# Optimization experiments

Hardware: AMD Instinct MI355X
Metric: run time of the kernel (lower is better)

The kernel has to match this reference:

```python
import jax, jax.numpy as jnp
import numpy as np

FUSE_W = 0.3
TEMP = 0.1
TOPK = 8
EPS = 1e-8


def _l2n(x, eps=EPS):
    return x / (jnp.linalg.norm(x, axis=-1, keepdims=True) + eps)


def setup_inputs() -> dict:
    key = jax.random.key(0)
    ks = jax.random.split(key, 6)
    B, Dk, Dv, N = 4096, 512, 512, 65536
    return {
        "q": jax.random.normal(ks[0], (B, Dk), jnp.float32),
        "spike_key": (jax.random.uniform(ks[1], (B, Dk)) > 0.5).astype(jnp.float32),
        "mem_keys": jax.random.normal(ks[2], (N, Dk), jnp.float32),
        "mem_values": jax.random.normal(ks[3], (N, Dv), jnp.float32),
        "W": jax.random.normal(ks[4], (Dk, Dk), jnp.float32) / np.sqrt(Dk).astype(np.float32),
        "b": jnp.zeros((Dk,), jnp.float32),
    }


def reference(q, spike_key, mem_keys, mem_values, W, b):
    # MemoryCube.query with spike fusion; memory fully filled (N = capacity).
    qn = _l2n(q)                                    # (B, Dk)
    enc = spike_key @ W.T + b                       # spike_encoder Linear
    qn = _l2n((1.0 - FUSE_W) * qn + FUSE_W * enc)   # _fuse_key
    keys_n = _l2n(mem_keys)                         # (N, Dk)
    sims = qn @ keys_n.T                            # (B, N) cosine sims
    top_vals, top_idx = jax.lax.top_k(sims, TOPK)   # (B, K)
    attn = jax.nn.softmax(top_vals / TEMP, axis=-1)
    vals = mem_values[top_idx]                      # (B, K, Dv) gather
    out = jnp.einsum('bk,bkd->bd', attn, vals)      # weighted combine
    # entropy-based confidence
    p = jnp.clip(attn, EPS, None)
    H = -(p * jnp.log(p)).sum(axis=-1)
    H_max = jnp.log(jnp.float32(TOPK))
    conf = (1.0 - H / (H_max + EPS)).mean()
    return out, conf, top_idx, attn
```

## Files before the change

### kernel.cpp

```cpp
#include <hip/hip_runtime.h>
#include <stdint.h>
#include <math.h>

typedef unsigned short u16;
typedef __attribute__((ext_vector_type(2))) float floatx2;
typedef __attribute__((ext_vector_type(4))) float floatx4;
typedef __attribute__((ext_vector_type(4))) unsigned int uintx4;
typedef __attribute__((ext_vector_type(8))) __bf16 bf16x8;

#define B_ROWS 4096
#define DK 512
#define NKEYS 65536
#define NCHUNK 32
#define CHUNK (NKEYS / NCHUNK)
#define SLOTS 32
#define CAND_PER_ROW (NCHUNK * SLOTS)
#define THRESH 0.135f

#define CONF_OFF 2097152
#define IDX_OFF  2097153
#define ATTN_OFF (IDX_OFF + B_ROWS * 8)

__device__ __forceinline__ u16 f2bf(float x) {
    union { float f; unsigned int u; } v; v.f = x;
    unsigned int r = v.u + 0x7fffu + ((v.u >> 16) & 1u);
    return (u16)(r >> 16);
}

__device__ __forceinline__ void gload_lds16(const u16* g, u16* l) {
    __builtin_amdgcn_global_load_lds(
        (const __attribute__((address_space(1))) unsigned int*)g,
        (__attribute__((address_space(3))) unsigned int*)l,
        16, 0, 0);
}

__device__ __forceinline__ float np_block128_sq(const float* a) {
#pragma clang fp contract(off)
    float r[8];
    floatx4 p0 = *(const floatx4*)&a[0];
    floatx4 p1 = *(const floatx4*)&a[4];
    r[0] = p0.x * p0.x; r[1] = p0.y * p0.y; r[2] = p0.z * p0.z; r[3] = p0.w * p0.w;
    r[4] = p1.x * p1.x; r[5] = p1.y * p1.y; r[6] = p1.z * p1.z; r[7] = p1.w * p1.w;
    for (int i = 8; i < 128; i += 8) {
        floatx4 q0 = *(const floatx4*)&a[i];
        floatx4 q1 = *(const floatx4*)&a[i + 4];
        r[0] += q0.x * q0.x; r[1] += q0.y * q0.y;
        r[2] += q0.z * q0.z; r[3] += q0.w * q0.w;
        r[4] += q1.x * q1.x; r[5] += q1.y * q1.y;
        r[6] += q1.z * q1.z; r[7] += q1.w * q1.w;
    }
    return ((r[0] + r[1]) + (r[2] + r[3])) + ((r[4] + r[5]) + (r[6] + r[7]));
}

__device__ __forceinline__ float np_sum512_sq(const float* a) {
#pragma clang fp contract(off)
    float b0 = np_block128_sq(a);
    float b1 = np_block128_sq(a + 128);
    float b2 = np_block128_sq(a + 256);
    float b3 = np_block128_sq(a + 384);
    return (b0 + b1) + (b2 + b3);
}

__device__ __forceinline__ float sqrt_f32_cr(float s) {
    return (float)sqrt((double)s);
}
__device__ __forceinline__ float div_f32_cr(float a, float b) {
    return (float)((double)a / (double)b);
}

__global__ __launch_bounds__(256) void transpose_w(const float* __restrict__ w,
                                                   float* __restrict__ wt) {
    int j = blockIdx.x, t = threadIdx.x;
    float a = w[(size_t)j * DK + t];
    float b = w[(size_t)j * DK + t + 256];
    wt[(size_t)t * DK + j] = a;
    wt[(size_t)(t + 256) * DK + j] = b;
}

__global__ __launch_bounds__(256) void prep_keys(float* __restrict__ mk,
                                                 u16* __restrict__ kbf) {
    const int row = blockIdx.x * 256 + threadIdx.x;
    float* kp = mk + (size_t)row * DK;
    float s = np_sum512_sq(kp);
    float nrm = sqrt_f32_cr(s) + 1e-8f;
    for (int i = 0; i < DK; i += 8) {
        floatx4 p0 = *(const floatx4*)&kp[i];
        floatx4 p1 = *(const floatx4*)&kp[i + 4];
        floatx4 n0, n1;
        n0.x = div_f32_cr(p0.x, nrm); n0.y = div_f32_cr(p0.y, nrm);
        n0.z = div_f32_cr(p0.z, nrm); n0.w = div_f32_cr(p0.w, nrm);
        n1.x = div_f32_cr(p1.x, nrm); n1.y = div_f32_cr(p1.y, nrm);
        n1.z = div_f32_cr(p1.z, nrm); n1.w = div_f32_cr(p1.w, nrm);
        union { uintx4 v; u16 u[8]; } pk;
        pk.u[0] = f2bf(n0.x); pk.u[1] = f2bf(n0.y);
        pk.u[2] = f2bf(n0.z); pk.u[3] = f2bf(n0.w);
        pk.u[4] = f2bf(n1.x); pk.u[5] = f2bf(n1.y);
        pk.u[6] = f2bf(n1.z); pk.u[7] = f2bf(n1.w);
        *(floatx4*)&kp[i] = n0;
        *(floatx4*)&kp[i + 4] = n1;
        *(uintx4*)&kbf[(size_t)row * DK + i] = pk.v;
    }
}

__global__ __launch_bounds__(256) void fuse_q(const float* __restrict__ q,
                                              const float* __restrict__ spike,
                                              const float* __restrict__ wt,
                                              const float* __restrict__ bvec,
                                              float* __restrict__ qn2f,
                                              u16* __restrict__ qbf) {
    __shared__ __align__(16) float s_sp[DK];
    __shared__ __align__(16) float s_q[DK];
    __shared__ __align__(16) float s_y[DK];
    __shared__ float s_nq;
    __shared__ float s_ny;
    const int t = threadIdx.x, b = blockIdx.x;
    s_sp[t] = spike[(size_t)b * DK + t];
    s_sp[t + 256] = spike[(size_t)b * DK + t + 256];
    s_q[t] = q[(size_t)b * DK + t];
    s_q[t + 256] = q[(size_t)b * DK + t + 256];
    __syncthreads();

    const int c0 = 2 * t;
    float a0 = 0.f, a1 = 0.f;
    for (int i = 0; i < DK; i += 16) {
        float sv[16]; floatx2 wv[16];
#pragma unroll
        for (int u = 0; u < 16; ++u) {
            sv[u] = s_sp[i + u];
            wv[u] = *(const floatx2*)&wt[(size_t)(i + u) * DK + c0];
        }
#pragma unroll
        for (int u = 0; u < 16; ++u) {
            a0 = fmaf(sv[u], wv[u].x, a0);
            a1 = fmaf(sv[u], wv[u].y, a1);
        }
    }

    if (t == 0) s_nq = sqrt_f32_cr(np_sum512_sq(s_q)) + 1e-8f;
    __syncthreads();
    float nq = s_nq;
    float qn0 = div_f32_cr(s_q[c0], nq);
    float qn1 = div_f32_cr(s_q[c0 + 1], nq);
    float e0 = a0 + bvec[c0];
    float e1 = a1 + bvec[c0 + 1];
    float y0, y1;
    {
#pragma clang fp contract(off)
        float u0 = 0.7f * qn0; float v0 = 0.3f * e0; y0 = u0 + v0;
        float u1 = 0.7f * qn1; float v1 = 0.3f * e1; y1 = u1 + v1;
    }
    s_y[c0] = y0; s_y[c0 + 1] = y1;
    __syncthreads();
    if (t == 0) s_ny = sqrt_f32_cr(np_sum512_sq(s_y)) + 1e-8f;
    __syncthreads();
    float ny = s_ny;
    float f0 = div_f32_cr(y0, ny);
    float f1 = div_f32_cr(y1, ny);
    *(floatx2*)&qn2f[(size_t)b * DK + c0] = (floatx2){f0, f1};
    union { unsigned int u; u16 h[2]; } pk;
    pk.h[0] = f2bf(f0); pk.h[1] = f2bf(f1);
    *(unsigned int*)&qbf[(size_t)b * DK + c0] = pk.u;
}

__global__ __launch_bounds__(256, 4) void cand_gemm(const u16* __restrict__ qbf,
                                                    const u16* __restrict__ kbf,
                                                    int* __restrict__ cidx,
                                                    int* __restrict__ gcnt) {
    __shared__ u16 ldsB[2][128 * 64];
    const int t = threadIdx.x;
    const int lane = t & 63;
    const int wave = t >> 6;
    const int qbase = blockIdx.x * 128;
    const int chunk = blockIdx.y;
    const int r0 = 64 * (wave >> 1), c0 = 64 * (wave & 1);
    const int quad = lane >> 4, m16 = lane & 15;

    const int srow = lane >> 3;
    const int scol = ((lane & 7) ^ srow) << 3;

    const u16* aRow = qbf + (size_t)(qbase + r0 + m16) * DK + quad * 8;

    floatx4 acc[4][4];

    {
        const u16* bB = kbf + (size_t)(chunk * CHUNK + wave * 32 + srow) * DK + scol;
#pragma unroll
        for (int c = 0; c < 4; ++c)
            gload_lds16(bB + (size_t)c * 8 * DK, &ldsB[0][(wave * 4 + c) * 512]);
    }
    __syncthreads();

    int cur = 0;
    for (int s = 0; s < 128; ++s) {
        const int iter = s >> 3;
        const int ks = (s & 7) << 6;
        const int nbase = chunk * CHUNK + iter * 128;

        if ((s & 7) == 0) {
#pragma unroll
            for (int i = 0; i < 4; ++i)
#pragma unroll
                for (int j = 0; j < 4; ++j) acc[i][j] = (floatx4){0.f, 0.f, 0.f, 0.f};
        }

        bf16x8 afr[2][4];
#pragma unroll
        for (int h = 0; h < 2; ++h)
#pragma unroll
            for (int i = 0; i < 4; ++i)
                afr[h][i] = __builtin_bit_cast(bf16x8,
                    *(const uintx4*)(aRow + (size_t)i * 16 * DK + ks + h * 32));

        if (s < 127) {
            const int s2 = s + 1;
            const int nb2 = chunk * CHUNK + (s2 >> 3) * 128;
            const int ks2 = (s2 & 7) << 6;
            const u16* bB = kbf + (size_t)(nb2 + wave * 32 + srow) * DK + ks2 + scol;
#pragma unroll
            for (int c = 0; c < 4; ++c)
                gload_lds16(bB + (size_t)c * 8 * DK, &ldsB[cur ^ 1][(wave * 4 + c) * 512]);
        }

#pragma unroll
        for (int h = 0; h < 2; ++h) {
            const int cb = ((h * 4 + quad) ^ (m16 & 7)) << 4;
            bf16x8 bfr[4];
#pragma unroll
            for (int j = 0; j < 4; ++j)
                bfr[j] = __builtin_bit_cast(bf16x8,
                    *(const uintx4*)((const char*)&ldsB[cur][0] + (c0 + 16 * j + m16) * 128 + cb));
#pragma unroll
            for (int i = 0; i < 4; ++i)
#pragma unroll
                for (int j = 0; j < 4; ++j)
                    acc[i][j] = __builtin_amdgcn_mfma_f32_16x16x32_bf16(
                        afr[h][i], bfr[j], acc[i][j], 0, 0, 0);
        }

        if ((s & 7) == 7) {
#pragma unroll
            for (int i = 0; i < 4; ++i)
#pragma unroll
                for (int j = 0; j < 4; ++j) {
                    int col = nbase + c0 + 16 * j + m16;
#pragma unroll
                    for (int r = 0; r < 4; ++r) {
                        float v = acc[i][j][r];
                        if (v > THRESH) {
                            int grow = qbase + r0 + 16 * i + quad * 4 + r;
                            int slot = atomicAdd(&gcnt[grow * NCHUNK + chunk], 1);
                            if (slot < SLOTS)
                                cidx[(size_t)grow * CAND_PER_ROW + chunk * SLOTS + slot] = col;
                        }
                    }
                }
        }
        __syncthreads();
        cur ^= 1;
    }
}

__global__ __launch_bounds__(256) void finalize_rows(const int* __restrict__ cidx,
                                                     const int* __restrict__ gcnt,
                                                     const float* __restrict__ qn2f,
                                                     const float* __restrict__ keys_n,
                                                     const float* __restrict__ mem_values,
                                                     float* __restrict__ out,
                                                     double* __restrict__ confp) {
    __shared__ __align__(16) float s_q[DK];
    __shared__ int s_cnt[NCHUNK];
    __shared__ int s_kin[CAND_PER_ROW];
    __shared__ float s_dv[CAND_PER_ROW];
    __shared__ int s_di[CAND_PER_ROW];
    __shared__ int s_n;
    __shared__ float s_lv[64][8];
    __shared__ int s_li[64][8];
    __shared__ float s_tv[8];
    __shared__ int s_ti[8];
    __shared__ double s_attn[8];

    const int b = blockIdx.x, t = threadIdx.x, lane = t & 63, wave = t >> 6;
    s_q[t] = qn2f[(size_t)b * DK + t];
    s_q[t + 256] = qn2f[(size_t)b * DK + t + 256];
    if (t == 0) s_n = 0;
    if (t < NCHUNK) {
        int c = gcnt[b * NCHUNK + t];
        s_cnt[t] = c < SLOTS ? c : SLOTS;
    }
    __syncthreads();

    for (int s = t; s < CAND_PER_ROW; s += 256) {
        int ch = s >> 5, sl = s & 31;
        if (sl < s_cnt[ch]) {
            int pos = atomicAdd(&s_n, 1);
            s_kin[pos] = cidx[(size_t)b * CAND_PER_ROW + s];
        }
    }
    __syncthreads();
    const int n = s_n;

    for (int p = t; p < n; p += 256) {
        int ki = s_kin[p];
        const float* kp = keys_n + (size_t)ki * DK;
        float acc = 0.f;
        for (int i = 0; i < DK; i += 4) {
            floatx4 kv = *(const floatx4*)&kp[i];
            acc = fmaf(s_q[i + 0], kv.x, acc);
            acc = fmaf(s_q[i + 1], kv.y, acc);
            acc = fmaf(s_q[i + 2], kv.z, acc);
            acc = fmaf(s_q[i + 3], kv.w, acc);
        }
        s_dv[p] = acc;
        s_di[p] = ki;
    }
    __syncthreads();

    if (wave == 0) {
        float lv[8]; int li[8];
#pragma unroll
        for (int k = 0; k < 8; ++k) { lv[k] = -1e30f; li[k] = 0x7fffffff; }
        for (int p = lane; p < n; p += 64) {
            float v = s_dv[p];
            int ki = s_di[p];
            if (v > lv[7] || (v == lv[7] && ki < li[7])) {
                lv[7] = v; li[7] = ki;
#pragma unroll
                for (int k = 7; k > 0; --k) {
                    bool sw = (lv[k] > lv[k - 1]) ||
                              (lv[k] == lv[k - 1] && li[k] < li[k - 1]);
                    if (sw) {
                        float tv = lv[k]; lv[k] = lv[k - 1]; lv[k - 1] = tv;
                        int ti = li[k]; li[k] = li[k - 1]; li[k - 1] = ti;
                    }
                }
            }
        }
#pragma unroll
        for (int k = 0; k < 8; ++k) { s_lv[lane][k] = lv[k]; s_li[lane][k] = li[k]; }
    }
    __syncthreads();

    if (t == 0) {
        int head[64];
#pragma unroll
        for (int l = 0; l < 64; ++l) head[l] = 0;
        for (int k = 0; k < 8; ++k) {
            float bv = -2e30f; int bi = 0x7fffffff; int bl = 0;
            for (int l = 0; l < 64; ++l) {
                int h = head[l];
                float v = s_lv[l][h];
                int ki = s_li[l][h];
                if (v > bv || (v == bv && ki < bi)) { bv = v; bi = ki; bl = l; }
            }
            head[bl]++;
            s_tv[k] = bv;
            s_ti[k] = (bi == 0x7fffffff) ? 0 : bi;
        }
        double mx = (double)s_tv[0];
        double e[8], sum = 0.0;
#pragma unroll
        for (int k = 0; k < 8; ++k) {
            e[k] = exp(((double)s_tv[k] - mx) / 0.1);
            sum += e[k];
        }
        double H = 0.0;
#pragma unroll
        for (int k = 0; k < 8; ++k) {
            double pa = e[k] / sum;
            s_attn[k] = pa;
            double pc = pa < 1e-8 ? 1e-8 : pa;
            H -= pc * log(pc);
        }
        confp[b] = 1.0 - H / (log(8.0) + 1e-8);
    }
    __syncthreads();

    if (t < 8) {
        out[IDX_OFF + (size_t)b * 8 + t] = (float)s_ti[t];
        out[ATTN_OFF + (size_t)b * 8 + t] = (float)s_attn[t];
    }
    for (int c = t; c < DK; c += 256) {
        double a = 0.0;
#pragma unroll
        for (int k = 0; k < 8; ++k)
            a += s_attn[k] * (double)mem_values[(size_t)s_ti[k] * DK + c];
        out[(size_t)b * DK + c] = (float)a;
    }
}

__global__ __launch_bounds__(256) void conf_reduce(const double* __restrict__ confp,
                                                   float* __restrict__ out) {
    __shared__ double red[256];
    int t = threadIdx.x;
    double s = 0.0;
    for (int i = t; i < B_ROWS; i += 256) s += confp[i];
    red[t] = s;
    __syncthreads();
    for (int k = 128; k > 0; k >>= 1) {
        if (t < k) red[t] += red[t + k];
        __syncthreads();
    }
    if (t == 0) out[CONF_OFF] = (float)(red[0] / 4096.0);
}

extern "C" void kernel_launch(void* const* d_in, const int* in_sizes, int n_in,
                              void* d_out, int out_size, void* d_ws, size_t ws_size,
                              hipStream_t stream) {
    const float* q     = (const float*)d_in[0];
    const float* spike = (const float*)d_in[1];
    float*       mk    = (float*)d_in[2];
    const float* mv    = (const float*)d_in[3];
    const float* w     = (const float*)d_in[4];
    const float* bvec  = (const float*)d_in[5];
    float* out = (float*)d_out;
    char* ws = (char*)d_ws;

    u16*    qbf   = (u16*)   (ws);
    u16*    kbf   = (u16*)   (ws + (4ull  << 20));
    float*  qn2f  = (float*) (ws + (68ull << 20));
    int*    cidx  = (int*)   (ws + (76ull << 20));
    float*  wt    = (float*) (ws + (92ull << 20));
    int*    gcnt  = (int*)   (ws + (93ull << 20));
    double* confp = (double*)(ws + (94ull << 20));

    hipMemsetAsync(gcnt, 0, (size_t)B_ROWS * NCHUNK * sizeof(int), stream);

    transpose_w<<<512, 256, 0, stream>>>(w, wt);
    prep_keys<<<NKEYS / 256, 256, 0, stream>>>(mk, kbf);
    fuse_q<<<B_ROWS, 256, 0, stream>>>(q, spike, wt, bvec, qn2f, qbf);
    cand_gemm<<<dim3(B_ROWS / 128, NCHUNK), 256, 0, stream>>>(qbf, kbf, cidx, gcnt);
    finalize_rows<<<B_ROWS, 256, 0, stream>>>(cidx, gcnt, qn2f, mk, mv, out, confp);
    conf_reduce<<<1, 256, 0, stream>>>(confp, out);
}
```

Baseline: 1.624 ms.

## Stage query A tiles through double-buffered LDS in candidate GEMM

The candidate GEMM used to read query fragments for A straight from global memory on every k-step. It now loads them asynchronously into a double-buffered LDS tile with the same swizzle as the B tile, prefetched one step ahead alongside B. This is meant to hide global-load latency for A and let the four waves share each loaded A tile. In exchange LDS use per block doubles, and launch bounds drop from 4 to 2 blocks per CU, which lowers occupancy.

```diff
diff --git a/kernel.cpp b/kernel.cpp
--- a/kernel.cpp
+++ b/kernel.cpp
@@ -162,10 +162,11 @@
     *(unsigned int*)&qbf[(size_t)b * DK + c0] = pk.u;
 }
 
-__global__ __launch_bounds__(256, 4) void cand_gemm(const u16* __restrict__ qbf,
+__global__ __launch_bounds__(256, 2) void cand_gemm(const u16* __restrict__ qbf,
                                                     const u16* __restrict__ kbf,
                                                     int* __restrict__ cidx,
                                                     int* __restrict__ gcnt) {
+    __shared__ u16 ldsA[2][128 * 64];
     __shared__ u16 ldsB[2][128 * 64];
     const int t = threadIdx.x;
     const int lane = t & 63;
@@ -178,53 +179,53 @@
     const int srow = lane >> 3;
     const int scol = ((lane & 7) ^ srow) << 3;
 
-    const u16* aRow = qbf + (size_t)(qbase + r0 + m16) * DK + quad * 8;
+    const u16* aB0 = qbf + (size_t)(qbase + wave * 32 + srow) * DK + scol;
 
     floatx4 acc[4][4];
 
     {
         const u16* bB = kbf + (size_t)(chunk * CHUNK + wave * 32 + srow) * DK + scol;
 #pragma unroll
-        for (int c = 0; c < 4; ++c)
+        for (int c = 0; c < 4; ++c) {
+            gload_lds16(aB0 + (size_t)c * 8 * DK, &ldsA[0][(wave * 4 + c) * 512]);
             gload_lds16(bB + (size_t)c * 8 * DK, &ldsB[0][(wave * 4 + c) * 512]);
+        }
     }
     __syncthreads();
 
     int cur = 0;
     for (int s = 0; s < 128; ++s) {
-        const int iter = s >> 3;
-        const int ks = (s & 7) << 6;
-        const int nbase = chunk * CHUNK + iter * 128;
-
-        if ((s & 7) == 0) {
-#pragma unroll
-            for (int i = 0; i < 4; ++i)
-#pragma unroll
-                for (int j = 0; j < 4; ++j) acc[i][j] = (floatx4){0.f, 0.f, 0.f, 0.f};
-        }
-
-        bf16x8 afr[2][4];
-#pragma unroll
-        for (int h = 0; h < 2; ++h)
-#pragma unroll
-            for (int i = 0; i < 4; ++i)
-                afr[h][i] = __builtin_bit_cast(bf16x8,
-                    *(const uintx4*)(aRow + (size_t)i * 16 * DK + ks + h * 32));
+        const int kstep = s & 7;
+        const int nbase = chunk * CHUNK + (s >> 3) * 128;
 
         if (s < 127) {
             const int s2 = s + 1;
-            const int nb2 = chunk * CHUNK + (s2 >> 3) * 128;
             const int ks2 = (s2 & 7) << 6;
-            const u16* bB = kbf + (size_t)(nb2 + wave * 32 + srow) * DK + ks2 + scol;
-#pragma unroll
-            for (int c = 0; c < 4; ++c)
+            const u16* aB = aB0 + ks2;
+            const u16* bB = kbf + (size_t)(chunk * CHUNK + (s2 >> 3) * 128 +
+                                           wave * 32 + srow) * DK + ks2 + scol;
+#pragma unroll
+            for (int c = 0; c < 4; ++c) {
+                gload_lds16(aB + (size_t)c * 8 * DK, &ldsA[cur ^ 1][(wave * 4 + c) * 512]);
                 gload_lds16(bB + (size_t)c * 8 * DK, &ldsB[cur ^ 1][(wave * 4 + c) * 512]);
+            }
+        }
+
+        if (kstep == 0) {
+#pragma unroll
+            for (int i = 0; i < 4; ++i)
+#pragma unroll
+                for (int j = 0; j < 4; ++j) acc[i][j] = (floatx4){0.f, 0.f, 0.f, 0.f};
         }
 
 #pragma unroll
         for (int h = 0; h < 2; ++h) {
             const int cb = ((h * 4 + quad) ^ (m16 & 7)) << 4;
-            bf16x8 bfr[4];
+            bf16x8 afr[4], bfr[4];
+#pragma unroll
+            for (int i = 0; i < 4; ++i)
+                afr[i] = __builtin_bit_cast(bf16x8,
+                    *(const uintx4*)((const char*)&ldsA[cur][0] + (r0 + 16 * i + m16) * 128 + cb));
 #pragma unroll
             for (int j = 0; j < 4; ++j)
                 bfr[j] = __builtin_bit_cast(bf16x8,
@@ -234,10 +235,10 @@
 #pragma unroll
                 for (int j = 0; j < 4; ++j)
                     acc[i][j] = __builtin_amdgcn_mfma_f32_16x16x32_bf16(
-                        afr[h][i], bfr[j], acc[i][j], 0, 0, 0);
-        }
-
-        if ((s & 7) == 7) {
+                        afr[h * 0 + i], bfr[j], acc[i][j], 0, 0, 0);
+        }
+
+        if (kstep == 7) {
 #pragma unroll
             for (int i = 0; i < 4; ++i)
 #pragma unroll
```

Result: faster. 1.422 ms (-12.4%).
